# Kernel tuning notes

Measured on AMD Instinct MI355X. Metric: run time of the kernel, lower is better.

The kernel has to match this reference:

```python
import jax, jax.numpy as jnp
import numpy as np

IN_DIM = 512
OUT_DIM = 128


def setup_inputs() -> dict:
    key = jax.random.key(0)
    ks = jax.random.split(key, 10)
    B, H, W = 8, 64, 64
    s_in = 1.0 / np.sqrt(IN_DIM)
    s_out = 1.0 / np.sqrt(OUT_DIM)
    return {
        "x": jax.random.normal(ks[0], (B, IN_DIM, H, W), dtype=jnp.float32),
        "W_in": jax.random.normal(ks[1], (OUT_DIM, IN_DIM), dtype=jnp.float32) * s_in,
        "b_in": jax.random.normal(ks[2], (OUT_DIM,), dtype=jnp.float32) * s_in,
        "W_q": jax.random.normal(ks[3], (OUT_DIM, OUT_DIM), dtype=jnp.float32) * s_out,
        "b_q": jax.random.normal(ks[4], (OUT_DIM,), dtype=jnp.float32) * s_out,
        "W_k": jax.random.normal(ks[5], (OUT_DIM, OUT_DIM), dtype=jnp.float32) * s_out,
        "b_k": jax.random.normal(ks[6], (OUT_DIM,), dtype=jnp.float32) * s_out,
        "W_v": jax.random.normal(ks[7], (OUT_DIM, OUT_DIM), dtype=jnp.float32) * s_out,
        "b_v": jax.random.normal(ks[8], (OUT_DIM,), dtype=jnp.float32) * s_out,
        "gamma": jax.random.normal(ks[9], (1,), dtype=jnp.float32) * 0.1,
    }


def reference(x, W_in, b_in, W_q, b_q, W_k, b_k, W_v, b_v, gamma):
    # 1x1 input projection: (B, C_in, H, W) -> (B, C, H, W)
    x = jnp.einsum('bihw,oi->bohw', x, W_in) + b_in[None, :, None, None]
    B, C, H, W = x.shape
    N = H * W
    xf = x.reshape(B, C, N)
    # 1x1 convs on flattened spatial dim are per-token matmuls
    q = jnp.einsum('bcn,oc->bon', xf, W_q) + b_q[None, :, None]  # (B, C, N)
    k = jnp.einsum('bcn,oc->bon', xf, W_k) + b_k[None, :, None]
    v = jnp.einsum('bcn,oc->bon', xf, W_v) + b_v[None, :, None]
    # energy[b, n, m] = sum_c q[b, c, n] * k[b, c, m]   (no 1/sqrt(d) scaling)
    energy = jnp.einsum('bcn,bcm->bnm', q, k)
    attention = jax.nn.softmax(energy, axis=-1)  # (B, N, N)
    # out[b, c, n] = sum_m v[b, c, m] * attention[b, n, m]  (V @ A^T)
    out = jnp.einsum('bcm,bnm->bcn', v, attention).reshape(B, C, H, W)
    return gamma * out + x
```

## Files before the change

### kernel.cpp

```cpp
#include <hip/hip_runtime.h>


typedef __attribute__((ext_vector_type(4))) float f32x4;
typedef __attribute__((ext_vector_type(8))) short bf16x8;
typedef __attribute__((ext_vector_type(2))) unsigned int u32x2;
typedef __attribute__((ext_vector_type(4))) unsigned int u32x4;

#define MFMA16(a, b, c) __builtin_amdgcn_mfma_f32_16x16x32_bf16((a), (b), (c), 0, 0, 0)
#define LOG2E 1.44269504088896340736f
#define SOFTMAX_SHIFT 40.0f

#if __has_builtin(__builtin_amdgcn_exp2f)
#define EXP2F(x) __builtin_amdgcn_exp2f(x)
#else
#define EXP2F(x) exp2f(x)
#endif

__device__ __forceinline__ unsigned short f2bf(float f) {
  union { float f; unsigned int u; } v; v.f = f;
  unsigned int r = v.u + 0x7FFFu + ((v.u >> 16) & 1u);
  return (unsigned short)(r >> 16);
}

__device__ __forceinline__ unsigned int pkbf(float a, float b) {
  unsigned int ua = __float_as_uint(a) + 0x8000u;
  unsigned int ub = __float_as_uint(b) + 0x8000u;
  return __builtin_amdgcn_perm(ub, ua, 0x07060302u);
}

__device__ __forceinline__ void gload_lds16(const void* g, void* l) {
  __builtin_amdgcn_global_load_lds(
      (const __attribute__((address_space(1))) unsigned int*)(unsigned long long)g,
      (__attribute__((address_space(3))) unsigned int*)(unsigned int)(unsigned long long)l,
      16, 0, 0);
}

__global__ void cvt_w_kernel(const float* __restrict__ Win, const float* __restrict__ Wq,
                             const float* __restrict__ Wk, const float* __restrict__ Wv,
                             unsigned short* __restrict__ o) {
  int t = blockIdx.x * 256 + threadIdx.x;
  if (t < 65536)       o[t] = f2bf(Win[t]);
  else if (t < 81920)  o[t] = f2bf(Wq[t - 65536]);
  else if (t < 98304)  o[t] = f2bf(Wk[t - 81920]);
  else if (t < 114688) o[t] = f2bf(Wv[t - 98304]);
}

__global__ __launch_bounds__(512) void proj_kernel(
    const float* __restrict__ x, const unsigned short* __restrict__ Wb,
    const float* __restrict__ b_in, const float* __restrict__ bq,
    const float* __restrict__ bk, const float* __restrict__ bv,
    float* __restrict__ xf, unsigned short* __restrict__ qt,
    unsigned short* __restrict__ kt, unsigned short* __restrict__ vv) {
  __shared__ alignas(16) unsigned short xt[32 * 512];
  __shared__ alignas(16) unsigned short xt2[32 * 512];
  const int tid = threadIdx.x;
  const int w = tid >> 6, L = tid & 63, l15 = L & 15, qd = L >> 4;
  const int n0 = blockIdx.x * 128;
  const int b = blockIdx.y;
  const float* xb = x + (size_t)b * 512 * 4096;

  const int io = tid >> 5, nq = tid & 31;
  const int il0 = io * 8, kkA = io >> 2, qr = io & 3;
  const int nbA = nq >> 2;
  const int Lsw8 = (L ^ ((L >> 2) & 7)) * 8;

  f32x4 acc[8];
#pragma unroll
  for (int nb = 0; nb < 8; ++nb) acc[nb] = (f32x4){0.f, 0.f, 0.f, 0.f};

  for (int c4 = 0; c4 < 4; ++c4) {
    const int i0 = c4 * 128;
    __syncthreads();
    f32x4 xv[8];
#pragma unroll
    for (int r = 0; r < 8; ++r)
      xv[r] = *(const f32x4*)(xb + (size_t)(i0 + il0 + r) * 4096 + n0 + nq * 4);
#pragma unroll
    for (int j = 0; j < 4; ++j) {
      const int n15 = (nq & 3) * 4 + j;
      const int s = qr * 16 + n15;
      const int sp = s ^ ((s >> 2) & 7);
      u32x4 d = {pkbf(xv[0][j], xv[1][j]), pkbf(xv[2][j], xv[3][j]),
                 pkbf(xv[4][j], xv[5][j]), pkbf(xv[6][j], xv[7][j])};
      *(u32x4*)&xt[(nbA * 4 + kkA) * 512 + sp * 8] = d;
    }
    __syncthreads();
#pragma unroll
    for (int kk = 0; kk < 4; ++kk) {
      bf16x8 a = *(const bf16x8*)(Wb + (size_t)(w * 16 + l15) * 512 + i0 + kk * 32 + qd * 8);
#pragma unroll
      for (int nb = 0; nb < 8; ++nb) {
        bf16x8 bfv = *(const bf16x8*)&xt[(nb * 4 + kk) * 512 + Lsw8];
        acc[nb] = MFMA16(a, bfv, acc[nb]);
      }
    }
  }
  {
    const int c0 = w * 16 + qd * 4;
    const float bi0 = b_in[c0], bi1 = b_in[c0 + 1], bi2 = b_in[c0 + 2], bi3 = b_in[c0 + 3];
    float* xfb = xf + (size_t)b * 128 * 4096;
    const int slot = ((w * 2 + (qd >> 1)) & 3) * 16 + l15;
    const int blkb = (w >> 1);
#pragma unroll
    for (int nb = 0; nb < 8; ++nb) {
      const int n = n0 + nb * 16 + l15;
      const float v0 = acc[nb][0] + bi0, v1 = acc[nb][1] + bi1;
      const float v2 = acc[nb][2] + bi2, v3 = acc[nb][3] + bi3;
      xfb[(size_t)(c0 + 0) * 4096 + n] = v0;
      xfb[(size_t)(c0 + 1) * 4096 + n] = v1;
      xfb[(size_t)(c0 + 2) * 4096 + n] = v2;
      xfb[(size_t)(c0 + 3) * 4096 + n] = v3;
      u32x2 h = {pkbf(v0, v1), pkbf(v2, v3)};
      *(u32x2*)&xt2[(nb * 4 + blkb) * 512 + slot * 8 + (qd & 1) * 4] = h;
    }
  }
  __syncthreads();

  for (int which = 0; which < 2; ++which) {
    const unsigned short* W = Wb + 65536 + which * 16384;
    const float* bias = which ? bk : bq;
    unsigned short* dst = (which ? kt : qt) + (size_t)b * 4096 * 128;
    f32x4 a2[8];
#pragma unroll
    for (int nb = 0; nb < 8; ++nb) a2[nb] = (f32x4){0.f, 0.f, 0.f, 0.f};
#pragma unroll
    for (int kk = 0; kk < 4; ++kk) {
      bf16x8 a = *(const bf16x8*)(W + (size_t)(w * 16 + l15) * 128 + kk * 32 + qd * 8);
#pragma unroll
      for (int nb = 0; nb < 8; ++nb) {
        bf16x8 bfv = *(const bf16x8*)&xt2[(nb * 4 + kk) * 512 + L * 8];
        a2[nb] = MFMA16(a, bfv, a2[nb]);
      }
    }
    const int c0 = w * 16 + qd * 4;
    const float b0 = bias[c0], b1 = bias[c0 + 1], b2 = bias[c0 + 2], b3 = bias[c0 + 3];
#pragma unroll
    for (int nb = 0; nb < 8; ++nb) {
      const int n = n0 + nb * 16 + l15;
      u32x2 h = {pkbf(a2[nb][0] + b0, a2[nb][1] + b1), pkbf(a2[nb][2] + b2, a2[nb][3] + b3)};
      *(u32x2*)&dst[(size_t)n * 128 + c0] = h;
    }
  }
  {
    const unsigned short* Wv = Wb + 98304;
    f32x4 a2[8];
#pragma unroll
    for (int cb = 0; cb < 8; ++cb) a2[cb] = (f32x4){0.f, 0.f, 0.f, 0.f};
#pragma unroll
    for (int kk = 0; kk < 4; ++kk) {
      bf16x8 a = *(const bf16x8*)&xt2[(w * 4 + kk) * 512 + L * 8];
#pragma unroll
      for (int cb = 0; cb < 8; ++cb) {
        bf16x8 bfv = *(const bf16x8*)(Wv + (size_t)(cb * 16 + l15) * 128 + kk * 32 + qd * 8);
        a2[cb] = MFMA16(a, bfv, a2[cb]);
      }
    }
    unsigned short* db = vv + (size_t)b * 128 * 4096;
    const int nbase = n0 + w * 16 + qd * 4;
#pragma unroll
    for (int cb = 0; cb < 8; ++cb) {
      const int c = cb * 16 + l15;
      const float bvv = bv[c];
      u32x2 h = {pkbf(a2[cb][0] + bvv, a2[cb][1] + bvv), pkbf(a2[cb][2] + bvv, a2[cb][3] + bvv)};
      *(u32x2*)&db[(size_t)c * 4096 + nbase] = h;
    }
  }
}

__global__ __launch_bounds__(256, 2) void attn_kernel(
    const unsigned short* __restrict__ qt, const unsigned short* __restrict__ kt,
    const unsigned short* __restrict__ vv, float* __restrict__ pa,
    float* __restrict__ lp, int nsplit) {
  __shared__ alignas(16) unsigned short kbuf[16 * 512];
  __shared__ alignas(16) unsigned short vbuf[16 * 512];
  __shared__ alignas(16) unsigned short pbuf[4][32][72];

  const int tid = threadIdx.x;
  const int w = tid >> 6, L = tid & 63, l15 = L & 15, qd = L >> 4;
  const int bidx = blockIdx.x;
  const int b = bidx & 7;
  const int r2 = bidx >> 3;
  const int qtile = r2 & 31, split = r2 >> 5;
  const int n00 = qtile * 128;
  const int mlen = 4096 / nsplit;
  const int mbeg = split * mlen;

  const unsigned short* qtb = qt + (size_t)b * 4096 * 128;
  const unsigned short* ktb = kt + (size_t)b * 4096 * 128;
  const unsigned short* vvb = vv + (size_t)b * 128 * 4096;

  bf16x8 qf[2][4];
#pragma unroll
  for (int nh = 0; nh < 2; ++nh) {
    const unsigned short* qrow = qtb + (size_t)(n00 + w * 32 + nh * 16 + l15) * 128 + qd * 8;
#pragma unroll
    for (int kk = 0; kk < 4; ++kk) qf[nh][kk] = *(const bf16x8*)(qrow + kk * 32);
  }

  f32x4 acc[2][8];
#pragma unroll
  for (int nh = 0; nh < 2; ++nh)
#pragma unroll
    for (int cb = 0; cb < 8; ++cb) acc[nh][cb] = (f32x4){0.f, 0.f, 0.f, 0.f};
  float lsum[2] = {0.f, 0.f};
  const float sb = SOFTMAX_SHIFT * LOG2E;

  for (int m0 = mbeg; m0 < mbeg + mlen; m0 += 64) {
    __syncthreads();
#pragma unroll
    for (int j = 0; j < 4; ++j) {
      const int blk = w * 4 + j;
      const int mb = blk >> 2, kk = blk & 3;
      gload_lds16(ktb + (size_t)(m0 + mb * 16 + l15) * 128 + kk * 32 + qd * 8,
                  &kbuf[blk * 512]);
      const int cb2 = blk >> 1, kkm = blk & 1;
      gload_lds16(vvb + (size_t)(cb2 * 16 + l15) * 4096 + m0 + kkm * 32 + qd * 8,
                  &vbuf[blk * 512]);
    }
    __syncthreads();

    f32x4 s[2][4];
#pragma unroll
    for (int mb = 0; mb < 4; ++mb) {
      s[0][mb] = (f32x4){0.f, 0.f, 0.f, 0.f};
      s[1][mb] = (f32x4){0.f, 0.f, 0.f, 0.f};
#pragma unroll
      for (int kk = 0; kk < 4; ++kk) {
        bf16x8 kf = *(const bf16x8*)&kbuf[(mb * 4 + kk) * 512 + L * 8];
        s[0][mb] = MFMA16(kf, qf[0][kk], s[0][mb]);
        s[1][mb] = MFMA16(kf, qf[1][kk], s[1][mb]);
      }
    }
#pragma unroll
    for (int nh = 0; nh < 2; ++nh) {
#pragma unroll
      for (int mb = 0; mb < 4; ++mb) {
        float p0 = EXP2F(__builtin_fmaf(s[nh][mb][0], LOG2E, -sb));
        float p1 = EXP2F(__builtin_fmaf(s[nh][mb][1], LOG2E, -sb));
        float p2 = EXP2F(__builtin_fmaf(s[nh][mb][2], LOG2E, -sb));
        float p3 = EXP2F(__builtin_fmaf(s[nh][mb][3], LOG2E, -sb));
        lsum[nh] += (p0 + p1) + (p2 + p3);
        u32x2 h = {pkbf(p0, p1), pkbf(p2, p3)};
        *(u32x2*)&pbuf[w][nh * 16 + l15][mb * 16 + qd * 4] = h;
      }
    }
#pragma unroll
    for (int kkm = 0; kkm < 2; ++kkm) {
      bf16x8 pf0 = *(const bf16x8*)&pbuf[w][l15][kkm * 32 + qd * 8];
      bf16x8 pf1 = *(const bf16x8*)&pbuf[w][16 + l15][kkm * 32 + qd * 8];
#pragma unroll
      for (int cb = 0; cb < 8; ++cb) {
        bf16x8 vf = *(const bf16x8*)&vbuf[(cb * 2 + kkm) * 512 + L * 8];
        acc[0][cb] = MFMA16(pf0, vf, acc[0][cb]);
        acc[1][cb] = MFMA16(pf1, vf, acc[1][cb]);
      }
    }
  }
#pragma unroll
  for (int nh = 0; nh < 2; ++nh) {
    lsum[nh] += __shfl_xor(lsum[nh], 16);
    lsum[nh] += __shfl_xor(lsum[nh], 32);
  }
  float* pab = pa + (size_t)(b * nsplit + split) * 4096 * 128;
#pragma unroll
  for (int nh = 0; nh < 2; ++nh) {
    const int nb_ = n00 + w * 32 + nh * 16 + qd * 4;
#pragma unroll
    for (int cb = 0; cb < 8; ++cb) {
      const int c = cb * 16 + l15;
#pragma unroll
      for (int r = 0; r < 4; ++r) pab[(size_t)(nb_ + r) * 128 + c] = acc[nh][cb][r];
    }
    if (L < 16) lp[(size_t)(b * nsplit + split) * 4096 + n00 + w * 32 + nh * 16 + l15] = lsum[nh];
  }
}

__global__ __launch_bounds__(256) void combine_kernel(
    const float* __restrict__ pa, const float* __restrict__ lp,
    const float* __restrict__ xf, const float* __restrict__ gamma_p,
    float* __restrict__ out, int nsplit) {
  __shared__ float tile[64 * 129];
  __shared__ float linv[64];
  const int tid = threadIdx.x;
  const int n0 = blockIdx.x * 64;
  const int b = blockIdx.y;

  const float* a0 = pa + ((size_t)(b * nsplit) * 4096 + n0) * 128;
#pragma unroll
  for (int i = 0; i < 8; ++i) {
    const int v = tid + i * 256;
    const int n = v >> 5, cw = (v & 31) * 4;
    f32x4 s = *(const f32x4*)(a0 + (size_t)n * 128 + cw);
    for (int sp = 1; sp < nsplit; ++sp)
      s += *(const f32x4*)(a0 + (size_t)sp * 4096 * 128 + (size_t)n * 128 + cw);
    float* t = &tile[n * 129 + cw];
    t[0] = s[0]; t[1] = s[1]; t[2] = s[2]; t[3] = s[3];
  }
  if (tid < 64) {
    float l = 0.f;
    for (int sp = 0; sp < nsplit; ++sp)
      l += lp[(size_t)(b * nsplit + sp) * 4096 + n0 + tid];
    linv[tid] = gamma_p[0] / l;
  }
  __syncthreads();
  const size_t ob = (size_t)b * 128 * 4096;
#pragma unroll
  for (int i = 0; i < 8; ++i) {
    const int v = tid + i * 256;
    const int c = v >> 4, nq = (v & 15) * 4;
    f32x4 xv = *(const f32x4*)(xf + ob + (size_t)c * 4096 + n0 + nq);
    f32x4 o;
#pragma unroll
    for (int j = 0; j < 4; ++j)
      o[j] = tile[(nq + j) * 129 + c] * linv[nq + j] + xv[j];
    *(f32x4*)(out + ob + (size_t)c * 4096 + n0 + nq) = o;
  }
}

extern "C" void kernel_launch(void* const* d_in, const int* in_sizes, int n_in,
                              void* d_out, int out_size, void* d_ws, size_t ws_size,
                              hipStream_t stream) {
  const float* x    = (const float*)d_in[0];
  const float* W_in = (const float*)d_in[1];
  const float* b_in = (const float*)d_in[2];
  const float* W_q  = (const float*)d_in[3];
  const float* b_q  = (const float*)d_in[4];
  const float* W_k  = (const float*)d_in[5];
  const float* b_k  = (const float*)d_in[6];
  const float* W_v  = (const float*)d_in[7];
  const float* b_v  = (const float*)d_in[8];
  const float* gam  = (const float*)d_in[9];
  float* out = (float*)d_out;

  char* ws = (char*)d_ws;
  unsigned short* Wb = (unsigned short*)ws;
  float* xf          = (float*)(ws + 262144);
  unsigned short* qt = (unsigned short*)(ws + 262144 + 16777216);
  unsigned short* kt = qt + (size_t)8 * 4096 * 128;
  unsigned short* vv = kt + (size_t)8 * 4096 * 128;
  const size_t base_end = 262144 + 16777216 + 3ull * 8388608;
  float* lp = (float*)(ws + base_end);
  float* pa = lp + (size_t)8 * 4 * 4096;

  const size_t fixed = base_end + 524288;
  const int nsplit = (ws_size >= fixed + 4ull * 16777216) ? 4
                   : (ws_size >= fixed + 2ull * 16777216) ? 2 : 1;

  cvt_w_kernel<<<448, 256, 0, stream>>>(W_in, W_q, W_k, W_v, Wb);
  proj_kernel<<<dim3(32, 8), 512, 0, stream>>>(x, Wb, b_in, b_q, b_k, b_v,
                                               xf, qt, kt, vv);
  attn_kernel<<<256 * nsplit, 256, 0, stream>>>(qt, kt, vv, pa, lp, nsplit);
  combine_kernel<<<dim3(64, 8), 256, 0, stream>>>(pa, lp, xf, gam, out, nsplit);
}
```

Measured before the change: 251.0 us.

## Stream V from global into registers, store bf16 partials, retile projection

The attention kernel now loads V fragments straight from global memory into registers instead of staging them in LDS. This removes the vbuf buffer and allows an occupancy hint of 3 blocks per CU. Split-K partial outputs are written as bf16 rather than fp32, halving partial-result traffic, and the combine kernel widens them back to fp32 when summing. The projection kernel is retiled to 64-token, 256-thread blocks with 2x4 MFMA tiles per warp. Risks are lower precision in the partial sums and global-load latency exposed inside the attention loop.

```diff
diff --git a/kernel.cpp b/kernel.cpp
--- a/kernel.cpp
+++ b/kernel.cpp
@@ -5,6 +5,7 @@
 typedef __attribute__((ext_vector_type(8))) short bf16x8;
 typedef __attribute__((ext_vector_type(2))) unsigned int u32x2;
 typedef __attribute__((ext_vector_type(4))) unsigned int u32x4;
+typedef __attribute__((ext_vector_type(4))) unsigned short u16x4;
 
 #define MFMA16(a, b, c) __builtin_amdgcn_mfma_f32_16x16x32_bf16((a), (b), (c), 0, 0, 0)
 #define LOG2E 1.44269504088896340736f
@@ -45,28 +46,30 @@
   else if (t < 114688) o[t] = f2bf(Wv[t - 98304]);
 }
 
-__global__ __launch_bounds__(512) void proj_kernel(
+__global__ __launch_bounds__(256) void proj_kernel(
     const float* __restrict__ x, const unsigned short* __restrict__ Wb,
     const float* __restrict__ b_in, const float* __restrict__ bq,
     const float* __restrict__ bk, const float* __restrict__ bv,
     float* __restrict__ xf, unsigned short* __restrict__ qt,
     unsigned short* __restrict__ kt, unsigned short* __restrict__ vv) {
-  __shared__ alignas(16) unsigned short xt[32 * 512];
-  __shared__ alignas(16) unsigned short xt2[32 * 512];
+  __shared__ alignas(16) unsigned short xt[16 * 512];
+  __shared__ alignas(16) unsigned short xt2[16 * 512];
   const int tid = threadIdx.x;
   const int w = tid >> 6, L = tid & 63, l15 = L & 15, qd = L >> 4;
-  const int n0 = blockIdx.x * 128;
+  const int n0 = blockIdx.x * 64;
   const int b = blockIdx.y;
   const float* xb = x + (size_t)b * 512 * 4096;
 
-  const int io = tid >> 5, nq = tid & 31;
+  const int io = tid >> 4, nq = tid & 15;
   const int il0 = io * 8, kkA = io >> 2, qr = io & 3;
   const int nbA = nq >> 2;
   const int Lsw8 = (L ^ ((L >> 2) & 7)) * 8;
 
-  f32x4 acc[8];
-#pragma unroll
-  for (int nb = 0; nb < 8; ++nb) acc[nb] = (f32x4){0.f, 0.f, 0.f, 0.f};
+  f32x4 acc[2][4];
+#pragma unroll
+  for (int ma = 0; ma < 2; ++ma)
+#pragma unroll
+    for (int nb = 0; nb < 4; ++nb) acc[ma][nb] = (f32x4){0.f, 0.f, 0.f, 0.f};
 
   for (int c4 = 0; c4 < 4; ++c4) {
     const int i0 = c4 * 128;
@@ -87,31 +90,38 @@
     __syncthreads();
 #pragma unroll
     for (int kk = 0; kk < 4; ++kk) {
-      bf16x8 a = *(const bf16x8*)(Wb + (size_t)(w * 16 + l15) * 512 + i0 + kk * 32 + qd * 8);
-#pragma unroll
-      for (int nb = 0; nb < 8; ++nb) {
+      bf16x8 a[2];
+#pragma unroll
+      for (int ma = 0; ma < 2; ++ma)
+        a[ma] = *(const bf16x8*)(Wb + (size_t)(w * 32 + ma * 16 + l15) * 512 + i0 + kk * 32 + qd * 8);
+#pragma unroll
+      for (int nb = 0; nb < 4; ++nb) {
         bf16x8 bfv = *(const bf16x8*)&xt[(nb * 4 + kk) * 512 + Lsw8];
-        acc[nb] = MFMA16(a, bfv, acc[nb]);
+#pragma unroll
+        for (int ma = 0; ma < 2; ++ma) acc[ma][nb] = MFMA16(a[ma], bfv, acc[ma][nb]);
       }
     }
   }
   {
-    const int c0 = w * 16 + qd * 4;
-    const float bi0 = b_in[c0], bi1 = b_in[c0 + 1], bi2 = b_in[c0 + 2], bi3 = b_in[c0 + 3];
     float* xfb = xf + (size_t)b * 128 * 4096;
-    const int slot = ((w * 2 + (qd >> 1)) & 3) * 16 + l15;
-    const int blkb = (w >> 1);
-#pragma unroll
-    for (int nb = 0; nb < 8; ++nb) {
-      const int n = n0 + nb * 16 + l15;
-      const float v0 = acc[nb][0] + bi0, v1 = acc[nb][1] + bi1;
-      const float v2 = acc[nb][2] + bi2, v3 = acc[nb][3] + bi3;
-      xfb[(size_t)(c0 + 0) * 4096 + n] = v0;
-      xfb[(size_t)(c0 + 1) * 4096 + n] = v1;
-      xfb[(size_t)(c0 + 2) * 4096 + n] = v2;
-      xfb[(size_t)(c0 + 3) * 4096 + n] = v3;
-      u32x2 h = {pkbf(v0, v1), pkbf(v2, v3)};
-      *(u32x2*)&xt2[(nb * 4 + blkb) * 512 + slot * 8 + (qd & 1) * 4] = h;
+#pragma unroll
+    for (int ma = 0; ma < 2; ++ma) {
+      const int c0 = w * 32 + ma * 16 + qd * 4;
+      const float bi0 = b_in[c0], bi1 = b_in[c0 + 1], bi2 = b_in[c0 + 2], bi3 = b_in[c0 + 3];
+      const int qdrow = ma * 2 + (qd >> 1);
+      const int joff = (qd & 1) * 4;
+#pragma unroll
+      for (int nb = 0; nb < 4; ++nb) {
+        const int n = n0 + nb * 16 + l15;
+        const float v0 = acc[ma][nb][0] + bi0, v1 = acc[ma][nb][1] + bi1;
+        const float v2 = acc[ma][nb][2] + bi2, v3 = acc[ma][nb][3] + bi3;
+        xfb[(size_t)(c0 + 0) * 4096 + n] = v0;
+        xfb[(size_t)(c0 + 1) * 4096 + n] = v1;
+        xfb[(size_t)(c0 + 2) * 4096 + n] = v2;
+        xfb[(size_t)(c0 + 3) * 4096 + n] = v3;
+        u32x2 h = {pkbf(v0, v1), pkbf(v2, v3)};
+        *(u32x2*)&xt2[(nb * 4 + w) * 512 + qdrow * 128 + l15 * 8 + joff] = h;
+      }
     }
   }
   __syncthreads();
@@ -120,25 +130,35 @@
     const unsigned short* W = Wb + 65536 + which * 16384;
     const float* bias = which ? bk : bq;
     unsigned short* dst = (which ? kt : qt) + (size_t)b * 4096 * 128;
-    f32x4 a2[8];
-#pragma unroll
-    for (int nb = 0; nb < 8; ++nb) a2[nb] = (f32x4){0.f, 0.f, 0.f, 0.f};
+    f32x4 a2[2][4];
+#pragma unroll
+    for (int ma = 0; ma < 2; ++ma)
+#pragma unroll
+      for (int nb = 0; nb < 4; ++nb) a2[ma][nb] = (f32x4){0.f, 0.f, 0.f, 0.f};
 #pragma unroll
     for (int kk = 0; kk < 4; ++kk) {
-      bf16x8 a = *(const bf16x8*)(W + (size_t)(w * 16 + l15) * 128 + kk * 32 + qd * 8);
-#pragma unroll
-      for (int nb = 0; nb < 8; ++nb) {
+      bf16x8 a[2];
+#pragma unroll
+      for (int ma = 0; ma < 2; ++ma)
+        a[ma] = *(const bf16x8*)(W + (size_t)(w * 32 + ma * 16 + l15) * 128 + kk * 32 + qd * 8);
+#pragma unroll
+      for (int nb = 0; nb < 4; ++nb) {
         bf16x8 bfv = *(const bf16x8*)&xt2[(nb * 4 + kk) * 512 + L * 8];
-        a2[nb] = MFMA16(a, bfv, a2[nb]);
-      }
-    }
-    const int c0 = w * 16 + qd * 4;
-    const float b0 = bias[c0], b1 = bias[c0 + 1], b2 = bias[c0 + 2], b3 = bias[c0 + 3];
-#pragma unroll
-    for (int nb = 0; nb < 8; ++nb) {
-      const int n = n0 + nb * 16 + l15;
-      u32x2 h = {pkbf(a2[nb][0] + b0, a2[nb][1] + b1), pkbf(a2[nb][2] + b2, a2[nb][3] + b3)};
-      *(u32x2*)&dst[(size_t)n * 128 + c0] = h;
+#pragma unroll
+        for (int ma = 0; ma < 2; ++ma) a2[ma][nb] = MFMA16(a[ma], bfv, a2[ma][nb]);
+      }
+    }
+#pragma unroll
+    for (int ma = 0; ma < 2; ++ma) {
+      const int c0 = w * 32 + ma * 16 + qd * 4;
+      const float b0 = bias[c0], b1 = bias[c0 + 1], b2 = bias[c0 + 2], b3 = bias[c0 + 3];
+#pragma unroll
+      for (int nb = 0; nb < 4; ++nb) {
+        const int n = n0 + nb * 16 + l15;
+        u32x2 h = {pkbf(a2[ma][nb][0] + b0, a2[ma][nb][1] + b1),
+                   pkbf(a2[ma][nb][2] + b2, a2[ma][nb][3] + b3)};
+        *(u32x2*)&dst[(size_t)n * 128 + c0] = h;
+      }
     }
   }
   {
@@ -167,12 +187,11 @@
   }
 }
 
-__global__ __launch_bounds__(256, 2) void attn_kernel(
+__global__ __launch_bounds__(256, 3) void attn_kernel(
     const unsigned short* __restrict__ qt, const unsigned short* __restrict__ kt,
-    const unsigned short* __restrict__ vv, float* __restrict__ pa,
+    const unsigned short* __restrict__ vv, unsigned short* __restrict__ pa,
     float* __restrict__ lp, int nsplit) {
   __shared__ alignas(16) unsigned short kbuf[16 * 512];
-  __shared__ alignas(16) unsigned short vbuf[16 * 512];
   __shared__ alignas(16) unsigned short pbuf[4][32][72];
 
   const int tid = threadIdx.x;
@@ -213,11 +232,14 @@
       const int mb = blk >> 2, kk = blk & 3;
       gload_lds16(ktb + (size_t)(m0 + mb * 16 + l15) * 128 + kk * 32 + qd * 8,
                   &kbuf[blk * 512]);
-      const int cb2 = blk >> 1, kkm = blk & 1;
-      gload_lds16(vvb + (size_t)(cb2 * 16 + l15) * 4096 + m0 + kkm * 32 + qd * 8,
-                  &vbuf[blk * 512]);
     }
     __syncthreads();
+
+    const unsigned short* vrow = vvb + (size_t)l15 * 4096 + m0 + qd * 8;
+    bf16x8 vf0[8];
+#pragma unroll
+    for (int cb = 0; cb < 8; ++cb)
+      vf0[cb] = *(const bf16x8*)(vrow + (size_t)cb * 16 * 4096);
 
     f32x4 s[2][4];
 #pragma unroll
@@ -244,15 +266,27 @@
         *(u32x2*)&pbuf[w][nh * 16 + l15][mb * 16 + qd * 4] = h;
       }
     }
-#pragma unroll
-    for (int kkm = 0; kkm < 2; ++kkm) {
-      bf16x8 pf0 = *(const bf16x8*)&pbuf[w][l15][kkm * 32 + qd * 8];
-      bf16x8 pf1 = *(const bf16x8*)&pbuf[w][16 + l15][kkm * 32 + qd * 8];
+    bf16x8 vf1[8];
+#pragma unroll
+    for (int cb = 0; cb < 8; ++cb)
+      vf1[cb] = *(const bf16x8*)(vrow + (size_t)cb * 16 * 4096 + 32);
+
+    {
+      bf16x8 pf0 = *(const bf16x8*)&pbuf[w][l15][qd * 8];
+      bf16x8 pf1 = *(const bf16x8*)&pbuf[w][16 + l15][qd * 8];
 #pragma unroll
       for (int cb = 0; cb < 8; ++cb) {
-        bf16x8 vf = *(const bf16x8*)&vbuf[(cb * 2 + kkm) * 512 + L * 8];
-        acc[0][cb] = MFMA16(pf0, vf, acc[0][cb]);
-        acc[1][cb] = MFMA16(pf1, vf, acc[1][cb]);
+        acc[0][cb] = MFMA16(pf0, vf0[cb], acc[0][cb]);
+        acc[1][cb] = MFMA16(pf1, vf0[cb], acc[1][cb]);
+      }
+    }
+    {
+      bf16x8 pf0 = *(const bf16x8*)&pbuf[w][l15][32 + qd * 8];
+      bf16x8 pf1 = *(const bf16x8*)&pbuf[w][16 + l15][32 + qd * 8];
+#pragma unroll
+      for (int cb = 0; cb < 8; ++cb) {
+        acc[0][cb] = MFMA16(pf0, vf1[cb], acc[0][cb]);
+        acc[1][cb] = MFMA16(pf1, vf1[cb], acc[1][cb]);
       }
     }
   }
@@ -261,7 +295,7 @@
     lsum[nh] += __shfl_xor(lsum[nh], 16);
     lsum[nh] += __shfl_xor(lsum[nh], 32);
   }
-  float* pab = pa + (size_t)(b * nsplit + split) * 4096 * 128;
+  unsigned short* pab = pa + (size_t)(b * nsplit + split) * 4096 * 128;
 #pragma unroll
   for (int nh = 0; nh < 2; ++nh) {
     const int nb_ = n00 + w * 32 + nh * 16 + qd * 4;
@@ -269,14 +303,14 @@
     for (int cb = 0; cb < 8; ++cb) {
       const int c = cb * 16 + l15;
 #pragma unroll
-      for (int r = 0; r < 4; ++r) pab[(size_t)(nb_ + r) * 128 + c] = acc[nh][cb][r];
+      for (int r = 0; r < 4; ++r) pab[(size_t)(nb_ + r) * 128 + c] = f2bf(acc[nh][cb][r]);
     }
     if (L < 16) lp[(size_t)(b * nsplit + split) * 4096 + n00 + w * 32 + nh * 16 + l15] = lsum[nh];
   }
 }
 
 __global__ __launch_bounds__(256) void combine_kernel(
-    const float* __restrict__ pa, const float* __restrict__ lp,
+    const unsigned short* __restrict__ pa, const float* __restrict__ lp,
     const float* __restrict__ xf, const float* __restrict__ gamma_p,
     float* __restrict__ out, int nsplit) {
   __shared__ float tile[64 * 129];
@@ -285,14 +319,17 @@
   const int n0 = blockIdx.x * 64;
   const int b = blockIdx.y;
 
-  const float* a0 = pa + ((size_t)(b * nsplit) * 4096 + n0) * 128;
+  const unsigned short* a0 = pa + ((size_t)(b * nsplit) * 4096 + n0) * 128;
 #pragma unroll
   for (int i = 0; i < 8; ++i) {
     const int v = tid + i * 256;
     const int n = v >> 5, cw = (v & 31) * 4;
-    f32x4 s = *(const f32x4*)(a0 + (size_t)n * 128 + cw);
-    for (int sp = 1; sp < nsplit; ++sp)
-      s += *(const f32x4*)(a0 + (size_t)sp * 4096 * 128 + (size_t)n * 128 + cw);
+    f32x4 s = (f32x4){0.f, 0.f, 0.f, 0.f};
+    for (int sp = 0; sp < nsplit; ++sp) {
+      u16x4 h = *(const u16x4*)(a0 + (size_t)sp * 4096 * 128 + (size_t)n * 128 + cw);
+#pragma unroll
+      for (int j = 0; j < 4; ++j) s[j] += __uint_as_float((unsigned int)h[j] << 16);
+    }
     float* t = &tile[n * 129 + cw];
     t[0] = s[0]; t[1] = s[1]; t[2] = s[2]; t[3] = s[3];
   }
@@ -339,15 +376,15 @@
   unsigned short* kt = qt + (size_t)8 * 4096 * 128;
   unsigned short* vv = kt + (size_t)8 * 4096 * 128;
   const size_t base_end = 262144 + 16777216 + 3ull * 8388608;
-  float* lp = (float*)(ws + base_end);
-  float* pa = lp + (size_t)8 * 4 * 4096;
+  float* lp          = (float*)(ws + base_end);
+  unsigned short* pa = (unsigned short*)(ws + base_end + 524288);
 
   const size_t fixed = base_end + 524288;
-  const int nsplit = (ws_size >= fixed + 4ull * 16777216) ? 4
-                   : (ws_size >= fixed + 2ull * 16777216) ? 2 : 1;
+  const int nsplit = (ws_size >= fixed + 4ull * 8388608) ? 4
+                   : (ws_size >= fixed + 2ull * 8388608) ? 2 : 1;
 
   cvt_w_kernel<<<448, 256, 0, stream>>>(W_in, W_q, W_k, W_v, Wb);
-  proj_kernel<<<dim3(32, 8), 512, 0, stream>>>(x, Wb, b_in, b_q, b_k, b_v,
+  proj_kernel<<<dim3(64, 8), 256, 0, stream>>>(x, Wb, b_in, b_q, b_k, b_v,
                                                xf, qt, kt, vv);
   attn_kernel<<<256 * nsplit, 256, 0, stream>>>(qt, kt, vv, pa, lp, nsplit);
   combine_kernel<<<dim3(64, 8), 256, 0, stream>>>(pa, lp, xf, gam, out, nsplit);
```

Measured after the change: 351.4 us. +40.0%, slower.
